# Kernel tuning notes

Hardware: AMD Instinct MI355X
Metric: run time of the kernel (lower is better)

The kernel has to match this reference:

```python
import jax, jax.numpy as jnp
import numpy as np

HIDDEN = 2048
INNER = 1024
NUM_EXPERTS = 64
TOP_K = 8
T_TOKENS = 512


def setup_inputs() -> dict:
    key = jax.random.key(0)
    k_x, k_gw, k_gb, k_w1, k_w2 = jax.random.split(key, 5)
    x = jax.random.normal(k_x, (T_TOKENS, HIDDEN), dtype=jnp.float32)
    gate_w = jax.random.normal(k_gw, (NUM_EXPERTS, HIDDEN), dtype=jnp.float32) * 0.02
    gate_b = jax.random.normal(k_gb, (NUM_EXPERTS,), dtype=jnp.float32) * 0.02
    # fc1: fused gate+up, [E, 2*INNER, HIDDEN]; fc2: down, [E, HIDDEN, INNER]
    w1 = jax.random.normal(k_w1, (NUM_EXPERTS, 2 * INNER, HIDDEN), dtype=jnp.float32) * 0.02
    w2 = jax.random.normal(k_w2, (NUM_EXPERTS, HIDDEN, INNER), dtype=jnp.float32) * 0.02
    return {"x": x, "gate_w": gate_w, "gate_b": gate_b, "w1": w1, "w2": w2}


def reference(x, gate_w, gate_b, w1, w2):
    # Router: ReplicatedLinear with bias -> logits [T, E]
    logits = x @ gate_w.T + gate_b
    # FusedMoE default routing: softmax (fp32), top-k, renormalize
    probs = jax.nn.softmax(logits.astype(jnp.float32), axis=-1)
    topk_w, topk_idx = jax.lax.top_k(probs, TOP_K)          # [T, K]
    topk_w = topk_w / jnp.sum(topk_w, axis=-1, keepdims=True)
    T, E = probs.shape
    # Sparse combine weights scattered into a dense [T, E] matrix
    combine = jnp.zeros((T, E), dtype=topk_w.dtype)
    combine = combine.at[jnp.arange(T)[:, None], topk_idx].add(topk_w)
    # Expert MLPs (dense-over-experts reference; combine zeros out unrouted pairs)
    h = jnp.einsum('th,eih->tei', x, w1)                    # [T, E, 2*INNER]
    gate_h, up_h = h[..., :INNER], h[..., INNER:]
    act = jax.nn.gelu(gate_h, approximate=True) * up_h      # gelu_pytorch_tanh
    y = jnp.einsum('tei,ehi->teh', act, w2)                 # [T, E, HIDDEN]
    # Weighted scatter-combine back to tokens
    return jnp.einsum('te,teh->th', combine.astype(x.dtype), y)
```

## Files before the change

kernel.cpp:

```cpp
#include <hip/hip_runtime.h>
#include <hip/hip_bf16.h>

#define HIDDEN 2048
#define INNER  1024
#define NE     64
#define TOPK   8
#define NTOK   512

typedef float f32x4 __attribute__((ext_vector_type(4)));
typedef short bf16x8 __attribute__((ext_vector_type(8)));

static __device__ __forceinline__ unsigned short b16(float f) {
  return __builtin_bit_cast(unsigned short, __float2bfloat16(f));
}
static __device__ __forceinline__ unsigned int pk2(float lo, float hi) {
  return (unsigned)b16(lo) | ((unsigned)b16(hi) << 16);
}

__global__ __launch_bounds__(256) void gating_kernel(
    const float* __restrict__ x, const float* __restrict__ gw, const float* __restrict__ gb,
    int* __restrict__ ticket, int* __restrict__ counts, int* __restrict__ offsets,
    int* __restrict__ topk_e, float* __restrict__ topk_w,
    int* __restrict__ perm_tok, float* __restrict__ perm_wt,
    unsigned short* __restrict__ xb, float* __restrict__ out) {
  const int t = blockIdx.x;
  const int tid = threadIdx.x;
  const int lane = tid & 63, w = tid >> 6;

  {
    const float4* xi = (const float4*)(x + (size_t)t * HIDDEN);
    float4 v0 = xi[tid * 2], v1 = xi[tid * 2 + 1];
    ushort4 o0, o1;
    o0.x = b16(v0.x); o0.y = b16(v0.y); o0.z = b16(v0.z); o0.w = b16(v0.w);
    o1.x = b16(v1.x); o1.y = b16(v1.y); o1.z = b16(v1.z); o1.w = b16(v1.w);
    ushort4* xo = (ushort4*)(xb + (size_t)t * HIDDEN);
    xo[tid * 2] = o0; xo[tid * 2 + 1] = o1;
    f32x4 z = (f32x4)0.f;
    f32x4* orow = (f32x4*)(out + (size_t)t * HIDDEN);
    orow[tid * 2] = z; orow[tid * 2 + 1] = z;
  }

  const int e = tid >> 2, seg = tid & 3;
  const f32x4* gr = (const f32x4*)(gw + (size_t)e * HIDDEN);
  const f32x4* xr = (const f32x4*)(x + (size_t)t * HIDDEN);
  float acc = 0.f;
  #pragma unroll 8
  for (int k = 0; k < 128; ++k) {
    int idx = k * 4 + seg;
    f32x4 a = xr[idx], b = gr[idx];
    acc += a.x * b.x + a.y * b.y + a.z * b.z + a.w * b.w;
  }
  acc += __shfl_xor(acc, 1);
  acc += __shfl_xor(acc, 2);
  __shared__ float sP[NE];
  if (seg == 0) sP[e] = acc;
  __syncthreads();

  __shared__ float sW[TOPK];
  __shared__ int   sE[TOPK];
  if (w == 0) {
    float logit = gb[lane] + sP[lane];
    float m = logit;
    #pragma unroll
    for (int off = 32; off; off >>= 1) m = fmaxf(m, __shfl_xor(m, off));
    float p = __expf(logit - m);
    float s = p;
    #pragma unroll
    for (int off = 32; off; off >>= 1) s += __shfl_xor(s, off);
    p /= s;
    float myp = p;
    #pragma unroll
    for (int k = 0; k < TOPK; ++k) {
      float v = myp; int ei = lane;
      #pragma unroll
      for (int off = 32; off; off >>= 1) {
        float v2 = __shfl_xor(v, off); int e2 = __shfl_xor(ei, off);
        if (v2 > v || (v2 == v && e2 < ei)) { v = v2; ei = e2; }
      }
      if (lane == 0) { sW[k] = v; sE[k] = ei; }
      if (lane == ei) myp = -1.0f;
    }
  }
  __syncthreads();
  if (tid < TOPK) {
    float ss = 0.f;
    #pragma unroll
    for (int k = 0; k < TOPK; ++k) ss += sW[k];
    topk_e[t * TOPK + tid] = sE[tid];
    topk_w[t * TOPK + tid] = sW[tid] / ss;
  }

  __threadfence();
  __syncthreads();
  __shared__ int slast;
  if (tid == 0) {
    int old = atomicAdd(ticket, 1);
    slast = (old == (int)gridDim.x - 1);
  }
  __syncthreads();
  if (!slast) return;
  __threadfence();

  __shared__ int hcnt[NE], soff[NE], ccur[NE];
  if (tid < NE) hcnt[tid] = 0;
  __syncthreads();
  for (int i = tid; i < NTOK * TOPK; i += 256) atomicAdd(&hcnt[topk_e[i]], 1);
  __syncthreads();
  if (tid < NE) {
    int c = hcnt[tid];
    int s = c;
    #pragma unroll
    for (int off = 1; off < 64; off <<= 1) {
      int o = __shfl_up(s, off);
      if (tid >= off) s += o;
    }
    soff[tid] = s - c; ccur[tid] = 0;
    counts[tid] = c; offsets[tid] = s - c;
  }
  __syncthreads();
  for (int i = tid; i < NTOK * TOPK; i += 256) {
    int ee = topk_e[i];
    int p = atomicAdd(&ccur[ee], 1);
    int pos = soff[ee] + p;
    perm_tok[pos] = i >> 3;
    perm_wt[pos] = topk_w[i];
  }
}

__global__ __launch_bounds__(512, 4) void phase1_kernel(
    const unsigned short* __restrict__ xb, const float* __restrict__ w1,
    const int* __restrict__ offsets, const int* __restrict__ counts,
    const int* __restrict__ perm_tok, unsigned short* __restrict__ act) {
  const int e = blockIdx.y, c = blockIdx.x;
  const int n_e = counts[e];
  if (n_e == 0) return;
  const int off = offsets[e];
  const int tid = threadIdx.x;
  const int lane = tid & 63, wave = tid >> 6;
  const int mat = wave >> 2;
  const int wm  = (wave & 3) * 32;

  const int r32 = tid >> 4, l16 = tid & 15;
  const float* wg  = w1 + (size_t)e * (2 * INNER) * HIDDEN;
  const float* rp0 = wg + (size_t)(c * 64 + r32) * HIDDEN;
  const float* rp1 = rp0 + (size_t)32 * HIDDEN;
  const float* rp2 = rp0 + (size_t)INNER * HIDDEN;
  const float* rp3 = rp2 + (size_t)32 * HIDDEN;
  const int bidx0 = r32 * 16 + (((l16 >> 1) ^ (r32 & 7)) << 1) + (l16 & 1);

  const int ar0 = tid >> 3, ar1 = (tid >> 3) + 64;
  const int as = tid & 7;
  const int sxa = as ^ (ar0 & 7);

  __shared__ uint4 smem[2][2][128 * 8];
  __shared__ int stok[128];
  float (*sU)[68] = (float(*)[68])&smem[0][0][0];

  for (int m0 = 0; m0 < n_e; m0 += 128) {
    __syncthreads();
    if (tid < 128) {
      int idx = m0 + tid;
      stok[tid] = perm_tok[off + (idx < n_e ? idx : n_e - 1)];
    }
    __syncthreads();

    uint4 va0, va1; f32x4 vB0, vB1, vB2, vB3;
    va0 = *((const uint4*)(xb + (size_t)stok[ar0] * HIDDEN) + as);
    va1 = *((const uint4*)(xb + (size_t)stok[ar1] * HIDDEN) + as);
    vB0 = *((const f32x4*)rp0 + l16);
    vB1 = *((const f32x4*)rp1 + l16);
    vB2 = *((const f32x4*)rp2 + l16);
    vB3 = *((const f32x4*)rp3 + l16);

    f32x4 acc[2][4];
    #pragma unroll
    for (int i = 0; i < 2; ++i)
      #pragma unroll
      for (int j = 0; j < 4; ++j) acc[i][j] = (f32x4)0.f;

    for (int k0 = 0; k0 < HIDDEN; k0 += 64) {
      const int cur = (k0 >> 6) & 1;
      smem[cur][0][ar0 * 8 + sxa] = va0;
      smem[cur][0][ar1 * 8 + sxa] = va1;
      {
        uint2* b2 = (uint2*)smem[cur][1];
        b2[bidx0]        = make_uint2(pk2(vB0.x, vB0.y), pk2(vB0.z, vB0.w));
        b2[bidx0 + 512]  = make_uint2(pk2(vB1.x, vB1.y), pk2(vB1.z, vB1.w));
        b2[bidx0 + 1024] = make_uint2(pk2(vB2.x, vB2.y), pk2(vB2.z, vB2.w));
        b2[bidx0 + 1536] = make_uint2(pk2(vB3.x, vB3.y), pk2(vB3.z, vB3.w));
      }
      __syncthreads();
      int k1 = k0 + 64;
      if (k1 < HIDDEN) {
        va0 = *((const uint4*)(xb + (size_t)stok[ar0] * HIDDEN + k1) + as);
        va1 = *((const uint4*)(xb + (size_t)stok[ar1] * HIDDEN + k1) + as);
        vB0 = *((const f32x4*)(rp0 + k1) + l16);
        vB1 = *((const f32x4*)(rp1 + k1) + l16);
        vB2 = *((const f32x4*)(rp2 + k1) + l16);
        vB3 = *((const f32x4*)(rp3 + k1) + l16);
      }
      #pragma unroll
      for (int ks = 0; ks < 2; ++ks) {
        const int u = ks * 4 + (lane >> 4);
        bf16x8 af[2], bfr[4];
        #pragma unroll
        for (int mi = 0; mi < 2; ++mi) {
          int r = wm + mi * 16 + (lane & 15);
          af[mi] = __builtin_bit_cast(bf16x8, smem[cur][0][r * 8 + (u ^ (r & 7))]);
        }
        #pragma unroll
        for (int ni = 0; ni < 4; ++ni) {
          int r = mat * 64 + ni * 16 + (lane & 15);
          bfr[ni] = __builtin_bit_cast(bf16x8, smem[cur][1][r * 8 + (u ^ (r & 7))]);
        }
        #pragma unroll
        for (int mi = 0; mi < 2; ++mi)
          #pragma unroll
          for (int ni = 0; ni < 4; ++ni)
            acc[mi][ni] = __builtin_amdgcn_mfma_f32_16x16x32_bf16(af[mi], bfr[ni], acc[mi][ni], 0, 0, 0);
      }
    }

    __syncthreads();
    if (mat == 1) {
      #pragma unroll
      for (int mi = 0; mi < 2; ++mi)
        #pragma unroll
        for (int ni = 0; ni < 4; ++ni)
          #pragma unroll
          for (int r4 = 0; r4 < 4; ++r4)
            sU[wm + mi * 16 + (lane >> 4) * 4 + r4][ni * 16 + (lane & 15)] = acc[mi][ni][r4];
    }
    __syncthreads();
    if (mat == 0) {
      #pragma unroll
      for (int mi = 0; mi < 2; ++mi)
        #pragma unroll
        for (int r4 = 0; r4 < 4; ++r4) {
          int mrow = wm + mi * 16 + (lane >> 4) * 4 + r4;
          int m = m0 + mrow;
          if (m < n_e) {
            unsigned short* arow = act + (size_t)(off + m) * INNER + c * 64;
            #pragma unroll
            for (int ni = 0; ni < 4; ++ni) {
              int col = ni * 16 + (lane & 15);
              float g = acc[mi][ni][r4];
              float uu = sU[mrow][col];
              float ge = g / (1.0f + __expf(-1.5957691216057308f * (g + 0.044715f * g * g * g)));
              arow[col] = b16(ge * uu);
            }
          }
        }
    }
  }
}

__global__ __launch_bounds__(512, 4) void phase2_kernel(
    const unsigned short* __restrict__ act, const float* __restrict__ w2,
    const int* __restrict__ offsets, const int* __restrict__ counts,
    const int* __restrict__ perm_tok, const float* __restrict__ perm_wt,
    float* __restrict__ out) {
  const int e = blockIdx.y, c = blockIdx.x;
  const int n_e = counts[e];
  if (n_e == 0) return;
  const int off = offsets[e];
  const int tid = threadIdx.x;
  const int lane = tid & 63, wave = tid >> 6;
  const int wm = (wave & 3) * 32;
  const int wn = (wave >> 2) * 64;

  const int r32 = tid >> 4, l16 = tid & 15;
  const float* rp0 = w2 + ((size_t)e * HIDDEN + c * 128 + r32) * INNER;
  const float* rp1 = rp0 + (size_t)32 * INNER;
  const float* rp2 = rp0 + (size_t)64 * INNER;
  const float* rp3 = rp0 + (size_t)96 * INNER;
  const int bidx0 = r32 * 16 + (((l16 >> 1) ^ (r32 & 7)) << 1) + (l16 & 1);

  const int ar0 = tid >> 3, ar1 = (tid >> 3) + 64;
  const int as = tid & 7;
  const int sxa = as ^ (ar0 & 7);

  __shared__ uint4 smem[2][2][128 * 8];

  for (int m0 = 0; m0 < n_e; m0 += 128) {
    const unsigned short* a0 = act + (size_t)(off + (m0 + ar0 < n_e ? m0 + ar0 : n_e - 1)) * INNER;
    const unsigned short* a1 = act + (size_t)(off + (m0 + ar1 < n_e ? m0 + ar1 : n_e - 1)) * INNER;

    uint4 va0, va1; f32x4 vB0, vB1, vB2, vB3;
    va0 = *((const uint4*)a0 + as);
    va1 = *((const uint4*)a1 + as);
    vB0 = *((const f32x4*)rp0 + l16);
    vB1 = *((const f32x4*)rp1 + l16);
    vB2 = *((const f32x4*)rp2 + l16);
    vB3 = *((const f32x4*)rp3 + l16);

    f32x4 acc[2][4];
    #pragma unroll
    for (int i = 0; i < 2; ++i)
      #pragma unroll
      for (int j = 0; j < 4; ++j) acc[i][j] = (f32x4)0.f;

    for (int k0 = 0; k0 < INNER; k0 += 64) {
      const int cur = (k0 >> 6) & 1;
      smem[cur][0][ar0 * 8 + sxa] = va0;
      smem[cur][0][ar1 * 8 + sxa] = va1;
      {
        uint2* b2 = (uint2*)smem[cur][1];
        b2[bidx0]        = make_uint2(pk2(vB0.x, vB0.y), pk2(vB0.z, vB0.w));
        b2[bidx0 + 512]  = make_uint2(pk2(vB1.x, vB1.y), pk2(vB1.z, vB1.w));
        b2[bidx0 + 1024] = make_uint2(pk2(vB2.x, vB2.y), pk2(vB2.z, vB2.w));
        b2[bidx0 + 1536] = make_uint2(pk2(vB3.x, vB3.y), pk2(vB3.z, vB3.w));
      }
      __syncthreads();
      int k1 = k0 + 64;
      if (k1 < INNER) {
        va0 = *((const uint4*)(a0 + k1) + as);
        va1 = *((const uint4*)(a1 + k1) + as);
        vB0 = *((const f32x4*)(rp0 + k1) + l16);
        vB1 = *((const f32x4*)(rp1 + k1) + l16);
        vB2 = *((const f32x4*)(rp2 + k1) + l16);
        vB3 = *((const f32x4*)(rp3 + k1) + l16);
      }
      #pragma unroll
      for (int ks = 0; ks < 2; ++ks) {
        const int u = ks * 4 + (lane >> 4);
        bf16x8 af[2], bfr[4];
        #pragma unroll
        for (int mi = 0; mi < 2; ++mi) {
          int r = wm + mi * 16 + (lane & 15);
          af[mi] = __builtin_bit_cast(bf16x8, smem[cur][0][r * 8 + (u ^ (r & 7))]);
        }
        #pragma unroll
        for (int ni = 0; ni < 4; ++ni) {
          int r = wn + ni * 16 + (lane & 15);
          bfr[ni] = __builtin_bit_cast(bf16x8, smem[cur][1][r * 8 + (u ^ (r & 7))]);
        }
        #pragma unroll
        for (int mi = 0; mi < 2; ++mi)
          #pragma unroll
          for (int ni = 0; ni < 4; ++ni)
            acc[mi][ni] = __builtin_amdgcn_mfma_f32_16x16x32_bf16(af[mi], bfr[ni], acc[mi][ni], 0, 0, 0);
      }
    }

    #pragma unroll
    for (int mi = 0; mi < 2; ++mi)
      #pragma unroll
      for (int r4 = 0; r4 < 4; ++r4) {
        int mrow = wm + mi * 16 + (lane >> 4) * 4 + r4;
        int m = m0 + mrow;
        if (m < n_e) {
          int tok = perm_tok[off + m];
          float wt = perm_wt[off + m];
          float* orow = out + (size_t)tok * HIDDEN + c * 128 + wn;
          #pragma unroll
          for (int ni = 0; ni < 4; ++ni)
            atomicAdd(&orow[ni * 16 + (lane & 15)], wt * acc[mi][ni][r4]);
        }
      }
    __syncthreads();
  }
}

extern "C" void kernel_launch(void* const* d_in, const int* in_sizes, int n_in,
                              void* d_out, int out_size, void* d_ws, size_t ws_size,
                              hipStream_t stream) {
  const float* x  = (const float*)d_in[0];
  const float* gw = (const float*)d_in[1];
  const float* gb = (const float*)d_in[2];
  const float* w1 = (const float*)d_in[3];
  const float* w2 = (const float*)d_in[4];
  float* out = (float*)d_out;

  char* ws = (char*)d_ws;
  int*   ticket   = (int*)(ws + 0x000);
  int*   counts   = (int*)(ws + 0x100);
  int*   offsets  = (int*)(ws + 0x200);
  int*   topk_e   = (int*)(ws + 0x1000);
  float* topk_w   = (float*)(ws + 0x5000);
  int*   perm_tok = (int*)(ws + 0x9000);
  float* perm_wt  = (float*)(ws + 0xD000);
  unsigned short* xb  = (unsigned short*)(ws + 0x11000);
  unsigned short* act = (unsigned short*)(ws + 0x220000);

  hipMemsetAsync(ticket, 0, 0x40, stream);

  gating_kernel<<<NTOK, 256, 0, stream>>>(x, gw, gb, ticket, counts, offsets,
                                          topk_e, topk_w, perm_tok, perm_wt, xb, out);
  phase1_kernel<<<dim3(16, NE), 512, 0, stream>>>(xb, w1, offsets, counts, perm_tok, act);
  phase2_kernel<<<dim3(16, NE), 512, 0, stream>>>(act, w2, offsets, counts, perm_tok, perm_wt, out);
}
```

Before: 453.3 us.

## Replace atomic scatter-combine with per-slot buffer plus gather combine kernel; XCD-aware block mapping

Phase 2 now writes unweighted expert outputs to a per-slot fp32 buffer instead of doing weighted float atomicAdds into the output. A new combine kernel gathers the top-k slots per token through an inverse permutation and sums them with the routing weights. This removes contention and the need to zero the output first, at the cost of an extra 32MB write/read and one more launch. Blocks are also launched on a flat grid, and the block index is decoded so that each expert's column tiles share an XCD, which should improve L2 reuse of that expert's weights.

```diff
diff --git a/kernel.cpp b/kernel.cpp
--- a/kernel.cpp
+++ b/kernel.cpp
@@ -17,12 +17,18 @@
   return (unsigned)b16(lo) | ((unsigned)b16(hi) << 16);
 }
 
+static __device__ __forceinline__ void decode_ce(int flat, int& c, int& e) {
+  int xcd = flat & 7, s = flat >> 3;
+  c = s & 15;
+  e = ((s >> 4) << 3) | xcd;
+}
+
 __global__ __launch_bounds__(256) void gating_kernel(
     const float* __restrict__ x, const float* __restrict__ gw, const float* __restrict__ gb,
     int* __restrict__ ticket, int* __restrict__ counts, int* __restrict__ offsets,
     int* __restrict__ topk_e, float* __restrict__ topk_w,
-    int* __restrict__ perm_tok, float* __restrict__ perm_wt,
-    unsigned short* __restrict__ xb, float* __restrict__ out) {
+    int* __restrict__ perm_tok, int* __restrict__ invpos,
+    unsigned short* __restrict__ xb) {
   const int t = blockIdx.x;
   const int tid = threadIdx.x;
   const int lane = tid & 63, w = tid >> 6;
@@ -35,9 +41,6 @@
     o1.x = b16(v1.x); o1.y = b16(v1.y); o1.z = b16(v1.z); o1.w = b16(v1.w);
     ushort4* xo = (ushort4*)(xb + (size_t)t * HIDDEN);
     xo[tid * 2] = o0; xo[tid * 2 + 1] = o1;
-    f32x4 z = (f32x4)0.f;
-    f32x4* orow = (f32x4*)(out + (size_t)t * HIDDEN);
-    orow[tid * 2] = z; orow[tid * 2 + 1] = z;
   }
 
   const int e = tid >> 2, seg = tid & 3;
@@ -123,7 +126,7 @@
     int p = atomicAdd(&ccur[ee], 1);
     int pos = soff[ee] + p;
     perm_tok[pos] = i >> 3;
-    perm_wt[pos] = topk_w[i];
+    invpos[i] = pos;
   }
 }
 
@@ -131,7 +134,8 @@
     const unsigned short* __restrict__ xb, const float* __restrict__ w1,
     const int* __restrict__ offsets, const int* __restrict__ counts,
     const int* __restrict__ perm_tok, unsigned short* __restrict__ act) {
-  const int e = blockIdx.y, c = blockIdx.x;
+  int c, e;
+  decode_ce(blockIdx.x, c, e);
   const int n_e = counts[e];
   if (n_e == 0) return;
   const int off = offsets[e];
@@ -258,9 +262,9 @@
 __global__ __launch_bounds__(512, 4) void phase2_kernel(
     const unsigned short* __restrict__ act, const float* __restrict__ w2,
     const int* __restrict__ offsets, const int* __restrict__ counts,
-    const int* __restrict__ perm_tok, const float* __restrict__ perm_wt,
-    float* __restrict__ out) {
-  const int e = blockIdx.y, c = blockIdx.x;
+    float* __restrict__ ybuf) {
+  int c, e;
+  decode_ce(blockIdx.x, c, e);
   const int n_e = counts[e];
   if (n_e == 0) return;
   const int off = offsets[e];
@@ -350,16 +354,35 @@
         int mrow = wm + mi * 16 + (lane >> 4) * 4 + r4;
         int m = m0 + mrow;
         if (m < n_e) {
-          int tok = perm_tok[off + m];
-          float wt = perm_wt[off + m];
-          float* orow = out + (size_t)tok * HIDDEN + c * 128 + wn;
+          float* orow = ybuf + (size_t)(off + m) * HIDDEN + c * 128 + wn;
           #pragma unroll
           for (int ni = 0; ni < 4; ++ni)
-            atomicAdd(&orow[ni * 16 + (lane & 15)], wt * acc[mi][ni][r4]);
+            orow[ni * 16 + (lane & 15)] = acc[mi][ni][r4];
         }
       }
     __syncthreads();
   }
+}
+
+__global__ __launch_bounds__(256) void combine_kernel(const float* __restrict__ ybuf,
+                                                      const int* __restrict__ invpos,
+                                                      const float* __restrict__ topk_w,
+                                                      float* __restrict__ out) {
+  int t = blockIdx.x;
+  int tid = threadIdx.x;
+  int col = tid * 8;
+  f32x4 a0 = (f32x4)0.f, a1 = (f32x4)0.f;
+  #pragma unroll
+  for (int k = 0; k < TOPK; ++k) {
+    int p = invpos[t * TOPK + k];
+    float w = topk_w[t * TOPK + k];
+    const f32x4* yr = (const f32x4*)(ybuf + (size_t)p * HIDDEN + col);
+    f32x4 v0 = yr[0], v1 = yr[1];
+    a0 += w * v0;
+    a1 += w * v1;
+  }
+  f32x4* o = (f32x4*)(out + (size_t)t * HIDDEN + col);
+  o[0] = a0; o[1] = a1;
 }
 
 extern "C" void kernel_launch(void* const* d_in, const int* in_sizes, int n_in,
@@ -379,14 +402,16 @@
   int*   topk_e   = (int*)(ws + 0x1000);
   float* topk_w   = (float*)(ws + 0x5000);
   int*   perm_tok = (int*)(ws + 0x9000);
-  float* perm_wt  = (float*)(ws + 0xD000);
+  int*   invpos   = (int*)(ws + 0xD000);
   unsigned short* xb  = (unsigned short*)(ws + 0x11000);
   unsigned short* act = (unsigned short*)(ws + 0x220000);
+  float* ybuf         = (float*)(ws + 0xA20000);
 
   hipMemsetAsync(ticket, 0, 0x40, stream);
 
   gating_kernel<<<NTOK, 256, 0, stream>>>(x, gw, gb, ticket, counts, offsets,
-                                          topk_e, topk_w, perm_tok, perm_wt, xb, out);
-  phase1_kernel<<<dim3(16, NE), 512, 0, stream>>>(xb, w1, offsets, counts, perm_tok, act);
-  phase2_kernel<<<dim3(16, NE), 512, 0, stream>>>(act, w2, offsets, counts, perm_tok, perm_wt, out);
-}
+                                          topk_e, topk_w, perm_tok, invpos, xb);
+  phase1_kernel<<<1024, 512, 0, stream>>>(xb, w1, offsets, counts, perm_tok, act);
+  phase2_kernel<<<1024, 512, 0, stream>>>(act, w2, offsets, counts, ybuf);
+  combine_kernel<<<NTOK, 256, 0, stream>>>(ybuf, invpos, topk_w, out);
+}
```

Result: no change. 448.5 us (-1.1%).

## Fuse expert up-projection and down-projection into one kernel with split-K over inner dim

Applied to the files above, without the earlier changes.

Merges the two expert GEMM kernels into one. Each block owns one expert and a 128-wide slice of the inner dimension: it computes gate and up for that slice, applies GELU-mul into shared memory, then multiplies by the matching w2 slice across all hidden columns and atomically accumulates into the output. This drops the global activation buffer round trip and one launch. In exchange there are more atomics into out (eight partial contributions per output element per expert), 80KB of shared memory per block with lower occupancy, and a smaller grid of 512 blocks.

```diff
diff --git a/kernel.cpp b/kernel.cpp
--- a/kernel.cpp
+++ b/kernel.cpp
@@ -127,238 +127,198 @@
   }
 }
 
-__global__ __launch_bounds__(512, 4) void phase1_kernel(
+__global__ __launch_bounds__(512, 2) void fused_kernel(
     const unsigned short* __restrict__ xb, const float* __restrict__ w1,
+    const float* __restrict__ w2,
     const int* __restrict__ offsets, const int* __restrict__ counts,
-    const int* __restrict__ perm_tok, unsigned short* __restrict__ act) {
-  const int e = blockIdx.y, c = blockIdx.x;
+    const int* __restrict__ perm_tok, const float* __restrict__ perm_wt,
+    float* __restrict__ out) {
+  const int e = blockIdx.x >> 3, q = blockIdx.x & 7;
   const int n_e = counts[e];
   if (n_e == 0) return;
   const int off = offsets[e];
   const int tid = threadIdx.x;
   const int lane = tid & 63, wave = tid >> 6;
-  const int mat = wave >> 2;
-  const int wm  = (wave & 3) * 32;
+  const int u2 = lane >> 4, l15 = lane & 15;
+  const int wm = (wave & 1) * 64;
+  const int wn = (wave >> 1) * 32;
+
+  __shared__ uint4 smem4[81920 / 16];
+  char* smem = (char*)smem4;
+  __shared__ int   stok[128];
+  __shared__ float swt[128];
+
+  const int arow = tid >> 2, aslot = tid & 3;
+  const int brow = tid >> 1, bh = tid & 1;
+  const int asw = (arow >> 1) & 3;
+  const int bsw = (brow >> 1) & 3;
+  const float* w1g = w1 + ((size_t)e * 2 * INNER + (size_t)q * 128) * HIDDEN;
+  const float* brptr = (brow < 128)
+      ? w1g + (size_t)brow * HIDDEN
+      : w1g + ((size_t)INNER + (brow - 128)) * HIDDEN;
 
   const int r32 = tid >> 4, l16 = tid & 15;
-  const float* wg  = w1 + (size_t)e * (2 * INNER) * HIDDEN;
-  const float* rp0 = wg + (size_t)(c * 64 + r32) * HIDDEN;
-  const float* rp1 = rp0 + (size_t)32 * HIDDEN;
-  const float* rp2 = rp0 + (size_t)INNER * HIDDEN;
-  const float* rp3 = rp2 + (size_t)32 * HIDDEN;
   const int bidx0 = r32 * 16 + (((l16 >> 1) ^ (r32 & 7)) << 1) + (l16 & 1);
-
-  const int ar0 = tid >> 3, ar1 = (tid >> 3) + 64;
-  const int as = tid & 7;
-  const int sxa = as ^ (ar0 & 7);
-
-  __shared__ uint4 smem[2][2][128 * 8];
-  __shared__ int stok[128];
-  float (*sU)[68] = (float(*)[68])&smem[0][0][0];
+  const float* w2q = w2 + (size_t)e * HIDDEN * INNER + (size_t)q * 128;
 
   for (int m0 = 0; m0 < n_e; m0 += 128) {
     __syncthreads();
     if (tid < 128) {
       int idx = m0 + tid;
-      stok[tid] = perm_tok[off + (idx < n_e ? idx : n_e - 1)];
+      int cl = idx < n_e ? idx : n_e - 1;
+      stok[tid] = perm_tok[off + cl];
+      swt[tid] = perm_wt[off + cl];
     }
     __syncthreads();
 
-    uint4 va0, va1; f32x4 vB0, vB1, vB2, vB3;
-    va0 = *((const uint4*)(xb + (size_t)stok[ar0] * HIDDEN) + as);
-    va1 = *((const uint4*)(xb + (size_t)stok[ar1] * HIDDEN) + as);
-    vB0 = *((const f32x4*)rp0 + l16);
-    vB1 = *((const f32x4*)rp1 + l16);
-    vB2 = *((const f32x4*)rp2 + l16);
-    vB3 = *((const f32x4*)rp3 + l16);
-
-    f32x4 acc[2][4];
-    #pragma unroll
-    for (int i = 0; i < 2; ++i)
-      #pragma unroll
-      for (int j = 0; j < 4; ++j) acc[i][j] = (f32x4)0.f;
-
-    for (int k0 = 0; k0 < HIDDEN; k0 += 64) {
-      const int cur = (k0 >> 6) & 1;
-      smem[cur][0][ar0 * 8 + sxa] = va0;
-      smem[cur][0][ar1 * 8 + sxa] = va1;
-      {
-        uint2* b2 = (uint2*)smem[cur][1];
-        b2[bidx0]        = make_uint2(pk2(vB0.x, vB0.y), pk2(vB0.z, vB0.w));
-        b2[bidx0 + 512]  = make_uint2(pk2(vB1.x, vB1.y), pk2(vB1.z, vB1.w));
-        b2[bidx0 + 1024] = make_uint2(pk2(vB2.x, vB2.y), pk2(vB2.z, vB2.w));
-        b2[bidx0 + 1536] = make_uint2(pk2(vB3.x, vB3.y), pk2(vB3.z, vB3.w));
-      }
+    const unsigned short* axrow = xb + (size_t)stok[arow] * HIDDEN;
+    uint4 a_r = ((const uint4*)axrow)[aslot];
+    f32x4 b_r0, b_r1, b_r2, b_r3;
+    {
+      const f32x4* bp = (const f32x4*)brptr;
+      b_r0 = bp[bh]; b_r1 = bp[bh + 2]; b_r2 = bp[bh + 4]; b_r3 = bp[bh + 6];
+    }
+
+    f32x4 ag[4][2], au[4][2];
+    #pragma unroll
+    for (int i = 0; i < 4; ++i)
+      #pragma unroll
+      for (int j = 0; j < 2; ++j) { ag[i][j] = (f32x4)0.f; au[i][j] = (f32x4)0.f; }
+
+    for (int k0 = 0; k0 < HIDDEN; k0 += 32) {
+      char* buf = smem + ((k0 >> 5) & 1) * 24576;
+      uint4* A1 = (uint4*)buf;
+      char*  B1 = buf + 8192;
+      A1[arow * 4 + (aslot ^ asw)] = a_r;
+      *(uint2*)(B1 + brow * 64 + ((0 ^ bsw) << 4) + bh * 8) =
+          make_uint2(pk2(b_r0.x, b_r0.y), pk2(b_r0.z, b_r0.w));
+      *(uint2*)(B1 + brow * 64 + ((1 ^ bsw) << 4) + bh * 8) =
+          make_uint2(pk2(b_r1.x, b_r1.y), pk2(b_r1.z, b_r1.w));
+      *(uint2*)(B1 + brow * 64 + ((2 ^ bsw) << 4) + bh * 8) =
+          make_uint2(pk2(b_r2.x, b_r2.y), pk2(b_r2.z, b_r2.w));
+      *(uint2*)(B1 + brow * 64 + ((3 ^ bsw) << 4) + bh * 8) =
+          make_uint2(pk2(b_r3.x, b_r3.y), pk2(b_r3.z, b_r3.w));
       __syncthreads();
-      int k1 = k0 + 64;
+      int k1 = k0 + 32;
       if (k1 < HIDDEN) {
-        va0 = *((const uint4*)(xb + (size_t)stok[ar0] * HIDDEN + k1) + as);
-        va1 = *((const uint4*)(xb + (size_t)stok[ar1] * HIDDEN + k1) + as);
-        vB0 = *((const f32x4*)(rp0 + k1) + l16);
-        vB1 = *((const f32x4*)(rp1 + k1) + l16);
-        vB2 = *((const f32x4*)(rp2 + k1) + l16);
-        vB3 = *((const f32x4*)(rp3 + k1) + l16);
+        a_r = ((const uint4*)(axrow + k1))[aslot];
+        const f32x4* bp = (const f32x4*)(brptr + k1);
+        b_r0 = bp[bh]; b_r1 = bp[bh + 2]; b_r2 = bp[bh + 4]; b_r3 = bp[bh + 6];
+      }
+      bf16x8 af[4], bg[2], bu[2];
+      #pragma unroll
+      for (int mi = 0; mi < 4; ++mi) {
+        int r = wm + mi * 16 + l15;
+        af[mi] = __builtin_bit_cast(bf16x8, A1[r * 4 + (u2 ^ ((r >> 1) & 3))]);
+      }
+      #pragma unroll
+      for (int ni = 0; ni < 2; ++ni) {
+        int rg = wn + ni * 16 + l15;
+        int sw = u2 ^ ((rg >> 1) & 3);
+        bg[ni] = __builtin_bit_cast(bf16x8, *(uint4*)(B1 + rg * 64 + (sw << 4)));
+        bu[ni] = __builtin_bit_cast(bf16x8, *(uint4*)(B1 + (128 + rg) * 64 + (sw << 4)));
+      }
+      #pragma unroll
+      for (int mi = 0; mi < 4; ++mi)
+        #pragma unroll
+        for (int ni = 0; ni < 2; ++ni) {
+          ag[mi][ni] = __builtin_amdgcn_mfma_f32_16x16x32_bf16(af[mi], bg[ni], ag[mi][ni], 0, 0, 0);
+          au[mi][ni] = __builtin_amdgcn_mfma_f32_16x16x32_bf16(af[mi], bu[ni], au[mi][ni], 0, 0, 0);
+        }
+    }
+
+    {
+      char* actb = smem + 49152;
+      #pragma unroll
+      for (int mi = 0; mi < 4; ++mi)
+        #pragma unroll
+        for (int ni = 0; ni < 2; ++ni)
+          #pragma unroll
+          for (int r4 = 0; r4 < 4; ++r4) {
+            int row = wm + mi * 16 + u2 * 4 + r4;
+            int col = wn + ni * 16 + l15;
+            float g = ag[mi][ni][r4];
+            float u = au[mi][ni][r4];
+            float ge = g / (1.0f + __expf(-1.5957691216057308f * (g + 0.044715f * g * g * g)));
+            int boff = row * 256 + (((col >> 3) ^ (row & 7)) << 4) + (col & 7) * 2;
+            *(unsigned short*)(actb + boff) = b16(ge * u);
+          }
+    }
+    __syncthreads();
+
+    f32x4 w_r0, w_r1, w_r2, w_r3;
+    {
+      const float* p0 = w2q + (size_t)r32 * INNER + l16 * 4;
+      w_r0 = *(const f32x4*)(p0);
+      w_r1 = *(const f32x4*)(p0 + (size_t)32 * INNER);
+      w_r2 = *(const f32x4*)(p0 + (size_t)64 * INNER);
+      w_r3 = *(const f32x4*)(p0 + (size_t)96 * INNER);
+    }
+    f32x4 acc[4][2];
+    char* actb = smem + 49152;
+
+    for (int j = 0; j < 32; ++j) {
+      const int kk = j & 1, n0 = (j >> 1) * 128;
+      char* buf2 = smem + (j & 1) * 16384;
+      uint2* B2 = (uint2*)buf2;
+      B2[bidx0]        = make_uint2(pk2(w_r0.x, w_r0.y), pk2(w_r0.z, w_r0.w));
+      B2[bidx0 + 512]  = make_uint2(pk2(w_r1.x, w_r1.y), pk2(w_r1.z, w_r1.w));
+      B2[bidx0 + 1024] = make_uint2(pk2(w_r2.x, w_r2.y), pk2(w_r2.z, w_r2.w));
+      B2[bidx0 + 1536] = make_uint2(pk2(w_r3.x, w_r3.y), pk2(w_r3.z, w_r3.w));
+      __syncthreads();
+      if (j + 1 < 32) {
+        int kk1 = (j + 1) & 1, n01 = ((j + 1) >> 1) * 128;
+        const float* pn = w2q + (size_t)(n01 + r32) * INNER + kk1 * 64 + l16 * 4;
+        w_r0 = *(const f32x4*)(pn);
+        w_r1 = *(const f32x4*)(pn + (size_t)32 * INNER);
+        w_r2 = *(const f32x4*)(pn + (size_t)64 * INNER);
+        w_r3 = *(const f32x4*)(pn + (size_t)96 * INNER);
+      }
+      if (kk == 0) {
+        #pragma unroll
+        for (int i = 0; i < 4; ++i)
+          #pragma unroll
+          for (int jj = 0; jj < 2; ++jj) acc[i][jj] = (f32x4)0.f;
       }
       #pragma unroll
       for (int ks = 0; ks < 2; ++ks) {
-        const int u = ks * 4 + (lane >> 4);
-        bf16x8 af[2], bfr[4];
-        #pragma unroll
-        for (int mi = 0; mi < 2; ++mi) {
-          int r = wm + mi * 16 + (lane & 15);
-          af[mi] = __builtin_bit_cast(bf16x8, smem[cur][0][r * 8 + (u ^ (r & 7))]);
+        bf16x8 af2[4], bf2[2];
+        #pragma unroll
+        for (int mi = 0; mi < 4; ++mi) {
+          int r = wm + mi * 16 + l15;
+          int slot = (kk * 8 + ks * 4 + u2) ^ (r & 7);
+          af2[mi] = __builtin_bit_cast(bf16x8, *(uint4*)(actb + r * 256 + (slot << 4)));
         }
         #pragma unroll
-        for (int ni = 0; ni < 4; ++ni) {
-          int r = mat * 64 + ni * 16 + (lane & 15);
-          bfr[ni] = __builtin_bit_cast(bf16x8, smem[cur][1][r * 8 + (u ^ (r & 7))]);
+        for (int ni = 0; ni < 2; ++ni) {
+          int r = wn + ni * 16 + l15;
+          int slot = (ks * 4 + u2) ^ (r & 7);
+          bf2[ni] = __builtin_bit_cast(bf16x8, *(uint4*)(buf2 + r * 128 + (slot << 4)));
         }
         #pragma unroll
-        for (int mi = 0; mi < 2; ++mi)
+        for (int mi = 0; mi < 4; ++mi)
           #pragma unroll
-          for (int ni = 0; ni < 4; ++ni)
-            acc[mi][ni] = __builtin_amdgcn_mfma_f32_16x16x32_bf16(af[mi], bfr[ni], acc[mi][ni], 0, 0, 0);
-      }
-    }
-
-    __syncthreads();
-    if (mat == 1) {
-      #pragma unroll
-      for (int mi = 0; mi < 2; ++mi)
-        #pragma unroll
-        for (int ni = 0; ni < 4; ++ni)
+          for (int ni = 0; ni < 2; ++ni)
+            acc[mi][ni] = __builtin_amdgcn_mfma_f32_16x16x32_bf16(af2[mi], bf2[ni], acc[mi][ni], 0, 0, 0);
+      }
+      if (kk == 1) {
+        #pragma unroll
+        for (int mi = 0; mi < 4; ++mi)
           #pragma unroll
-          for (int r4 = 0; r4 < 4; ++r4)
-            sU[wm + mi * 16 + (lane >> 4) * 4 + r4][ni * 16 + (lane & 15)] = acc[mi][ni][r4];
-    }
-    __syncthreads();
-    if (mat == 0) {
-      #pragma unroll
-      for (int mi = 0; mi < 2; ++mi)
-        #pragma unroll
-        for (int r4 = 0; r4 < 4; ++r4) {
-          int mrow = wm + mi * 16 + (lane >> 4) * 4 + r4;
-          int m = m0 + mrow;
-          if (m < n_e) {
-            unsigned short* arow = act + (size_t)(off + m) * INNER + c * 64;
-            #pragma unroll
-            for (int ni = 0; ni < 4; ++ni) {
-              int col = ni * 16 + (lane & 15);
-              float g = acc[mi][ni][r4];
-              float uu = sU[mrow][col];
-              float ge = g / (1.0f + __expf(-1.5957691216057308f * (g + 0.044715f * g * g * g)));
-              arow[col] = b16(ge * uu);
+          for (int r4 = 0; r4 < 4; ++r4) {
+            int mrow = wm + mi * 16 + u2 * 4 + r4;
+            int m = m0 + mrow;
+            if (m < n_e) {
+              int tok = stok[mrow];
+              float wt = swt[mrow];
+              float* orow = out + (size_t)tok * HIDDEN + n0 + wn;
+              #pragma unroll
+              for (int ni = 0; ni < 2; ++ni)
+                atomicAdd(&orow[ni * 16 + l15], wt * acc[mi][ni][r4]);
             }
           }
-        }
-    }
-  }
-}
-
-__global__ __launch_bounds__(512, 4) void phase2_kernel(
-    const unsigned short* __restrict__ act, const float* __restrict__ w2,
-    const int* __restrict__ offsets, const int* __restrict__ counts,
-    const int* __restrict__ perm_tok, const float* __restrict__ perm_wt,
-    float* __restrict__ out) {
-  const int e = blockIdx.y, c = blockIdx.x;
-  const int n_e = counts[e];
-  if (n_e == 0) return;
-  const int off = offsets[e];
-  const int tid = threadIdx.x;
-  const int lane = tid & 63, wave = tid >> 6;
-  const int wm = (wave & 3) * 32;
-  const int wn = (wave >> 2) * 64;
-
-  const int r32 = tid >> 4, l16 = tid & 15;
-  const float* rp0 = w2 + ((size_t)e * HIDDEN + c * 128 + r32) * INNER;
-  const float* rp1 = rp0 + (size_t)32 * INNER;
-  const float* rp2 = rp0 + (size_t)64 * INNER;
-  const float* rp3 = rp0 + (size_t)96 * INNER;
-  const int bidx0 = r32 * 16 + (((l16 >> 1) ^ (r32 & 7)) << 1) + (l16 & 1);
-
-  const int ar0 = tid >> 3, ar1 = (tid >> 3) + 64;
-  const int as = tid & 7;
-  const int sxa = as ^ (ar0 & 7);
-
-  __shared__ uint4 smem[2][2][128 * 8];
-
-  for (int m0 = 0; m0 < n_e; m0 += 128) {
-    const unsigned short* a0 = act + (size_t)(off + (m0 + ar0 < n_e ? m0 + ar0 : n_e - 1)) * INNER;
-    const unsigned short* a1 = act + (size_t)(off + (m0 + ar1 < n_e ? m0 + ar1 : n_e - 1)) * INNER;
-
-    uint4 va0, va1; f32x4 vB0, vB1, vB2, vB3;
-    va0 = *((const uint4*)a0 + as);
-    va1 = *((const uint4*)a1 + as);
-    vB0 = *((const f32x4*)rp0 + l16);
-    vB1 = *((const f32x4*)rp1 + l16);
-    vB2 = *((const f32x4*)rp2 + l16);
-    vB3 = *((const f32x4*)rp3 + l16);
-
-    f32x4 acc[2][4];
-    #pragma unroll
-    for (int i = 0; i < 2; ++i)
-      #pragma unroll
-      for (int j = 0; j < 4; ++j) acc[i][j] = (f32x4)0.f;
-
-    for (int k0 = 0; k0 < INNER; k0 += 64) {
-      const int cur = (k0 >> 6) & 1;
-      smem[cur][0][ar0 * 8 + sxa] = va0;
-      smem[cur][0][ar1 * 8 + sxa] = va1;
-      {
-        uint2* b2 = (uint2*)smem[cur][1];
-        b2[bidx0]        = make_uint2(pk2(vB0.x, vB0.y), pk2(vB0.z, vB0.w));
-        b2[bidx0 + 512]  = make_uint2(pk2(vB1.x, vB1.y), pk2(vB1.z, vB1.w));
-        b2[bidx0 + 1024] = make_uint2(pk2(vB2.x, vB2.y), pk2(vB2.z, vB2.w));
-        b2[bidx0 + 1536] = make_uint2(pk2(vB3.x, vB3.y), pk2(vB3.z, vB3.w));
-      }
-      __syncthreads();
-      int k1 = k0 + 64;
-      if (k1 < INNER) {
-        va0 = *((const uint4*)(a0 + k1) + as);
-        va1 = *((const uint4*)(a1 + k1) + as);
-        vB0 = *((const f32x4*)(rp0 + k1) + l16);
-        vB1 = *((const f32x4*)(rp1 + k1) + l16);
-        vB2 = *((const f32x4*)(rp2 + k1) + l16);
-        vB3 = *((const f32x4*)(rp3 + k1) + l16);
-      }
-      #pragma unroll
-      for (int ks = 0; ks < 2; ++ks) {
-        const int u = ks * 4 + (lane >> 4);
-        bf16x8 af[2], bfr[4];
-        #pragma unroll
-        for (int mi = 0; mi < 2; ++mi) {
-          int r = wm + mi * 16 + (lane & 15);
-          af[mi] = __builtin_bit_cast(bf16x8, smem[cur][0][r * 8 + (u ^ (r & 7))]);
-        }
-        #pragma unroll
-        for (int ni = 0; ni < 4; ++ni) {
-          int r = wn + ni * 16 + (lane & 15);
-          bfr[ni] = __builtin_bit_cast(bf16x8, smem[cur][1][r * 8 + (u ^ (r & 7))]);
-        }
-        #pragma unroll
-        for (int mi = 0; mi < 2; ++mi)
-          #pragma unroll
-          for (int ni = 0; ni < 4; ++ni)
-            acc[mi][ni] = __builtin_amdgcn_mfma_f32_16x16x32_bf16(af[mi], bfr[ni], acc[mi][ni], 0, 0, 0);
-      }
-    }
-
-    #pragma unroll
-    for (int mi = 0; mi < 2; ++mi)
-      #pragma unroll
-      for (int r4 = 0; r4 < 4; ++r4) {
-        int mrow = wm + mi * 16 + (lane >> 4) * 4 + r4;
-        int m = m0 + mrow;
-        if (m < n_e) {
-          int tok = perm_tok[off + m];
-          float wt = perm_wt[off + m];
-          float* orow = out + (size_t)tok * HIDDEN + c * 128 + wn;
-          #pragma unroll
-          for (int ni = 0; ni < 4; ++ni)
-            atomicAdd(&orow[ni * 16 + (lane & 15)], wt * acc[mi][ni][r4]);
-        }
-      }
-    __syncthreads();
+      }
+    }
   }
 }
 
@@ -380,13 +340,12 @@
   float* topk_w   = (float*)(ws + 0x5000);
   int*   perm_tok = (int*)(ws + 0x9000);
   float* perm_wt  = (float*)(ws + 0xD000);
-  unsigned short* xb  = (unsigned short*)(ws + 0x11000);
-  unsigned short* act = (unsigned short*)(ws + 0x220000);
+  unsigned short* xb = (unsigned short*)(ws + 0x11000);
 
   hipMemsetAsync(ticket, 0, 0x40, stream);
 
   gating_kernel<<<NTOK, 256, 0, stream>>>(x, gw, gb, ticket, counts, offsets,
                                           topk_e, topk_w, perm_tok, perm_wt, xb, out);
-  phase1_kernel<<<dim3(16, NE), 512, 0, stream>>>(xb, w1, offsets, counts, perm_tok, act);
-  phase2_kernel<<<dim3(16, NE), 512, 0, stream>>>(act, w2, offsets, counts, perm_tok, perm_wt, out);
-}
+  fused_kernel<<<NE * 8, 512, 0, stream>>>(xb, w1, w2, offsets, counts,
+                                           perm_tok, perm_wt, out);
+}
```

Measured after the change: 553.1 us. +22.0%, slower.
